# Kernel optimization log

Measured on AMD Instinct MI355X. Metric: run time of the kernel, lower is better.

The kernel has to match this reference:

```python
import jax, jax.numpy as jnp
import numpy as np

D = 64          # d_model
H = 128         # ffn_hidden_dim
N = 10000       # nodes
E = 50000       # edges
NEG_SLOPE = 0.01  # LeakyReLU default


def setup_inputs() -> dict:
    key = jax.random.key(0)
    ks = jax.random.split(key, 10)
    x = jax.random.normal(ks[0], (N, D), dtype=jnp.float32)
    edge_index = jax.random.randint(ks[1], (2, E), 0, N)
    edge_attr = jax.random.normal(ks[2], (E, D), dtype=jnp.float32)
    # MapE2NxN params (stored as [in, out] so forward is x @ W + b)
    w1 = jax.random.normal(ks[3], (D, H), dtype=jnp.float32) / np.sqrt(D)
    b1 = jnp.zeros((H,), dtype=jnp.float32)
    w2 = jax.random.normal(ks[4], (H, D * D), dtype=jnp.float32) / np.sqrt(H)
    b2 = jnp.zeros((D * D,), dtype=jnp.float32)
    # NNConv root weight + bias
    root = jax.random.normal(ks[5], (D, D), dtype=jnp.float32) / np.sqrt(D)
    bias = jnp.zeros((D,), dtype=jnp.float32)
    # LayerNorm affine params
    gamma = jnp.ones((D,), dtype=jnp.float32)
    beta = jnp.zeros((D,), dtype=jnp.float32)
    return {"x": x, "edge_attr": edge_attr, "gamma": gamma, "beta": beta,
            "w1": w1, "b1": b1, "w2": w2, "b2": b2,
            "root": root, "bias": bias, "edge_index": edge_index}


def _layer_norm(h, gamma, beta, eps=1e-5):
    mu = jnp.mean(h, axis=-1, keepdims=True)
    var = jnp.var(h, axis=-1, keepdims=True)
    return (h - mu) * jax.lax.rsqrt(var + eps) * gamma + beta


def _leaky_relu(h):
    return jnp.where(h >= 0, h, NEG_SLOPE * h)


def reference(x, edge_attr, gamma, beta, w1, b1, w2, b2, root, bias, edge_index):
    src, dst = edge_index[0], edge_index[1]
    # DeepGCNLayer block='res+': pre-activation norm -> act -> (dropout p=0) -> conv -> residual
    h = _leaky_relu(_layer_norm(x, gamma, beta))
    # MapE2NxN on edge attributes -> per-edge [D, D] weight matrix
    we = _leaky_relu(edge_attr @ w1 + b1) @ w2 + b2   # [E, D*D]
    we = we.reshape(E, D, D)
    # per-edge matvec with source node features (PyG NNConv message)
    msg = jnp.einsum('ed,edf->ef', h[src], we)        # [E, D]
    # scatter-mean aggregate into destination nodes
    agg = jax.ops.segment_sum(msg, dst, num_segments=N)
    cnt = jax.ops.segment_sum(jnp.ones((E,), dtype=msg.dtype), dst, num_segments=N)
    agg = agg / jnp.maximum(cnt, 1.0)[:, None]
    # root transform + bias, then residual
    out = agg + h @ root + bias
    return x + out
```

## Files before the change

### kernel.cpp

```cpp
#include <hip/hip_runtime.h>

#define NS 10000
#define DD 64
#define HH 128
#define EE 50000
#define SLOPE 0.01f

typedef __attribute__((ext_vector_type(8))) short short8;
typedef __attribute__((ext_vector_type(4))) float f32x4;

static __device__ __forceinline__ unsigned short f2bf(float f) {
  unsigned int u = __float_as_uint(f);
  u += 0x7fff + ((u >> 16) & 1);
  return (unsigned short)(u >> 16);
}

__device__ __forceinline__ float wave_sum64(float v) {
  #pragma unroll
  for (int m = 32; m >= 1; m >>= 1) v += __shfl_xor(v, m, 64);
  return v;
}

#define TBLK 128
__global__ __launch_bounds__(256) void k_prep(const float* __restrict__ x,
    const float* __restrict__ gamma, const float* __restrict__ beta,
    float* __restrict__ h, unsigned short* __restrict__ hbf,
    const float* __restrict__ ea, unsigned short* __restrict__ eabf,
    const float* __restrict__ w2, unsigned short* __restrict__ w2t2,
    const float* __restrict__ w1, unsigned short* __restrict__ w1t,
    const float* __restrict__ b2, unsigned short* __restrict__ b2t,
    const int* __restrict__ ei, int* __restrict__ cntsrc,
    int* __restrict__ cntdst) {
  __shared__ float tile[64][65];
  int t = threadIdx.x;
  int bid = blockIdx.x;
  if (bid < TBLK) {
    int k = bid;
    #pragma unroll
    for (int i = 0; i < 16; ++i) {
      int idx = t + i * 256;
      tile[idx >> 6][idx & 63] = w2[k * (DD * DD) + idx];
    }
    __syncthreads();
    #pragma unroll
    for (int it = 0; it < 2; ++it) {
      int slot = t + it * 256;
      int f = slot >> 3, l8 = slot & 7;
      short8 o;
      #pragma unroll
      for (int j = 0; j < 8; ++j) o[j] = f2bf(tile[l8 * 8 + j][f]);
      *(short8*)(w2t2 + ((size_t)(f * HH + k)) * DD + l8 * 8) = o;
    }
    return;
  }
  int pbid = bid - TBLK;
  int gid = pbid * 256 + t;
  if (gid < EE) {
    atomicAdd(&cntsrc[ei[gid]], 1);
    atomicAdd(&cntdst[ei[EE + gid]], 1);
  }
  if (gid < EE * DD / 8) {
    const float4* sp = (const float4*)(ea + (size_t)gid * 8);
    float4 v0 = sp[0], v1 = sp[1];
    short8 o;
    o[0] = f2bf(v0.x); o[1] = f2bf(v0.y); o[2] = f2bf(v0.z); o[3] = f2bf(v0.w);
    o[4] = f2bf(v1.x); o[5] = f2bf(v1.y); o[6] = f2bf(v1.z); o[7] = f2bf(v1.w);
    *(short8*)(eabf + (size_t)gid * 8) = o;
  }
  if (gid < DD * HH) {
    int d = gid & 63, hc = gid >> 6;
    w1t[gid] = f2bf(w1[d * HH + hc]);
  }
  if (gid < DD * DD) {
    int d = gid & 63, f = gid >> 6;
    b2t[gid] = f2bf(b2[d * DD + f]);
  }
  int wid = t >> 6;
  int lane = t & 63;
  int row = pbid * 4 + wid;
  if (row >= NS) return;
  float v = x[row * DD + lane];
  float s = wave_sum64(v);
  float s2 = wave_sum64(v * v);
  float mu = s * (1.0f / 64.0f);
  float var = s2 * (1.0f / 64.0f) - mu * mu;
  float r = rsqrtf(var + 1e-5f);
  float hn = (v - mu) * r * gamma[lane] + beta[lane];
  float hv = hn >= 0.f ? hn : SLOPE * hn;
  h[row * DD + lane] = hv;
  hbf[row * DD + lane] = f2bf(hv);
}

#define UBLK 782
#define CBLK 157
#define TSTART 944
__global__ __launch_bounds__(256) void k_midT(
    const unsigned short* __restrict__ eabf, const unsigned short* __restrict__ w1t,
    const float* __restrict__ b1, unsigned short* __restrict__ ubf,
    const unsigned short* __restrict__ hbf, const unsigned short* __restrict__ b2t,
    float* __restrict__ cc, const int* __restrict__ cntsrc,
    int* __restrict__ rowptr, int* __restrict__ cursor,
    const unsigned short* __restrict__ w2t2, unsigned short* __restrict__ T,
    int n0, int n1, int gx, int doMid) {
  __shared__ unsigned short As[64][72];
  __shared__ unsigned short Bs[128 * 72];
  int t = threadIdx.x;
  int bid = blockIdx.x;
  int w = t >> 6, lane = t & 63, lr = lane & 15, lg = lane >> 4;
  if (bid < UBLK) {
    if (!doMid) return;
    int r0 = bid * 64 + w * 16;
    int ra = r0 + lr; if (ra >= EE) ra = EE - 1;
    short8 a0 = *(const short8*)(eabf + (size_t)ra * DD + lg * 8);
    short8 a1 = *(const short8*)(eabf + (size_t)ra * DD + 32 + lg * 8);
    short8 bb0[8], bb1[8];
    #pragma unroll
    for (int ni = 0; ni < 8; ++ni) {
      const unsigned short* bp = w1t + (ni * 16 + lr) * DD;
      bb0[ni] = *(const short8*)(bp + lg * 8);
      bb1[ni] = *(const short8*)(bp + 32 + lg * 8);
    }
    f32x4 acc[8] = {};
    #pragma unroll
    for (int ni = 0; ni < 8; ++ni) {
      acc[ni] = __builtin_amdgcn_mfma_f32_16x16x32_bf16(a0, bb0[ni], acc[ni], 0, 0, 0);
      acc[ni] = __builtin_amdgcn_mfma_f32_16x16x32_bf16(a1, bb1[ni], acc[ni], 0, 0, 0);
    }
    #pragma unroll
    for (int ni = 0; ni < 8; ++ni) {
      int col = ni * 16 + lr;
      float bb = b1[col];
      #pragma unroll
      for (int reg = 0; reg < 4; ++reg) {
        int gr = r0 + lg * 4 + reg;
        if (gr < EE) {
          float vv = acc[ni][reg] + bb;
          ubf[(size_t)gr * HH + col] = f2bf(vv >= 0.f ? vv : SLOPE * vv);
        }
      }
    }
    return;
  } else if (bid < UBLK + CBLK) {
    if (!doMid) return;
    int row0 = (bid - UBLK) * 64;
    short8 a[4][2];
    #pragma unroll
    for (int mi = 0; mi < 4; ++mi) {
      int ra = row0 + mi * 16 + lr; if (ra >= NS) ra = NS - 1;
      a[mi][0] = *(const short8*)(hbf + (size_t)ra * DD + lg * 8);
      a[mi][1] = *(const short8*)(hbf + (size_t)ra * DD + 32 + lg * 8);
    }
    const unsigned short* bp = b2t + (w * 16 + lr) * DD;
    short8 b0 = *(const short8*)(bp + lg * 8);
    short8 b1v = *(const short8*)(bp + 32 + lg * 8);
    f32x4 acc[4] = {};
    #pragma unroll
    for (int mi = 0; mi < 4; ++mi) {
      acc[mi] = __builtin_amdgcn_mfma_f32_16x16x32_bf16(a[mi][0], b0, acc[mi], 0, 0, 0);
      acc[mi] = __builtin_amdgcn_mfma_f32_16x16x32_bf16(a[mi][1], b1v, acc[mi], 0, 0, 0);
    }
    #pragma unroll
    for (int mi = 0; mi < 4; ++mi)
      #pragma unroll
      for (int reg = 0; reg < 4; ++reg) {
        int gr = row0 + mi * 16 + lg * 4 + reg;
        if (gr < NS) cc[(size_t)gr * DD + w * 16 + lr] = acc[mi][reg];
      }
    return;
  } else if (bid == UBLK + CBLK) {
    if (!doMid) return;
    int* ps = (int*)&As[0][0];
    const int CH = (NS + 255) / 256;
    int base = t * CH;
    int sum = 0;
    for (int i = 0; i < CH; ++i) {
      int idx = base + i;
      if (idx < NS) sum += cntsrc[idx];
    }
    ps[t] = sum;
    __syncthreads();
    for (int off = 1; off < 256; off <<= 1) {
      int v = (t >= off) ? ps[t - off] : 0;
      __syncthreads();
      ps[t] += v;
      __syncthreads();
    }
    int run = ps[t] - sum;
    for (int i = 0; i < CH; ++i) {
      int idx = base + i;
      if (idx < NS) {
        rowptr[idx] = run;
        cursor[idx] = run;
        run += cntsrc[idx];
      }
    }
    if (t == 255) rowptr[NS] = run;
    return;
  }
  if (bid < TSTART) return;
  int tb = bid - TSTART;
  int bx = tb % gx, by = tb / gx;
  int row0 = n0 + bx * 64;
  if (row0 >= n1) return;
  int col0 = by * 128;
  #pragma unroll
  for (int i = 0; i < 2; ++i) {
    int idx = t + i * 256;
    int r = idx >> 3, cc2 = (idx & 7) * 8;
    int gr = row0 + r;
    short8 v = {};
    if (gr < n1) v = *(const short8*)(hbf + (size_t)gr * DD + cc2);
    *(short8*)(&As[r][cc2]) = v;
  }
  #pragma unroll
  for (int i = 0; i < 4; ++i) {
    int idx = t + i * 256;
    int cL = idx >> 3, rr = (idx & 7) * 8;
    int gc = col0 + cL;
    short8 v = *(const short8*)(w2t2 + (size_t)gc * DD + rr);
    *(short8*)(&Bs[cL * 72 + rr]) = v;
  }
  __syncthreads();
  f32x4 acc[4][2] = {};
  #pragma unroll
  for (int kk = 0; kk < 64; kk += 32) {
    short8 a[4], b[2];
    #pragma unroll
    for (int mi = 0; mi < 4; ++mi)
      a[mi] = *(const short8*)(&As[mi * 16 + lr][kk + lg * 8]);
    #pragma unroll
    for (int ni = 0; ni < 2; ++ni)
      b[ni] = *(const short8*)(&Bs[(w * 32 + ni * 16 + lr) * 72 + kk + lg * 8]);
    #pragma unroll
    for (int mi = 0; mi < 4; ++mi)
      #pragma unroll
      for (int ni = 0; ni < 2; ++ni)
        acc[mi][ni] = __builtin_amdgcn_mfma_f32_16x16x32_bf16(
            a[mi], b[ni], acc[mi][ni], 0, 0, 0);
  }
  __syncthreads();
  #pragma unroll
  for (int mi = 0; mi < 4; ++mi)
    #pragma unroll
    for (int ni = 0; ni < 2; ++ni) {
      int col = w * 32 + ni * 16 + lr;
      #pragma unroll
      for (int reg = 0; reg < 4; ++reg)
        Bs[(mi * 16 + lg * 4 + reg) * 132 + col] = f2bf(acc[mi][ni][reg]);
    }
  __syncthreads();
  #pragma unroll
  for (int i = 0; i < 4; ++i) {
    int idx = t + i * 256;
    int row = idx >> 4, seg = idx & 15;
    int gr = row0 + row;
    if (gr < n1) {
      short8 v = *(const short8*)(&Bs[row * 132 + seg * 8]);
      *(short8*)(T + (size_t)(gr - n0) * (HH * DD) + col0 + seg * 8) = v;
    }
  }
}

__global__ __launch_bounds__(256) void k_scatter(const int* __restrict__ ei,
    int* __restrict__ cursor, int* __restrict__ eord) {
  int e = blockIdx.x * 256 + threadIdx.x;
  if (e < EE) {
    int s = ei[e];
    int pos = atomicAdd(&cursor[s], 1);
    eord[pos] = e;
  }
}

__global__ __launch_bounds__(256) void k_msg_wave(
    const unsigned short* __restrict__ ubf, const unsigned short* __restrict__ T,
    const float* __restrict__ cc, const int* __restrict__ ei,
    const int* __restrict__ rowptr, const int* __restrict__ eord,
    float* __restrict__ agg, int n0, int n1) {
  int wid = threadIdx.x >> 6;
  int lane = threadIdx.x & 63;
  int s = n0 + blockIdx.x * 64 + blockIdx.y * 4 + wid;
  if (s >= n1) return;
  int beg = rowptr[s];
  int deg = rowptr[s + 1] - beg;
  if (deg == 0) return;
  int lr = lane & 15, lg = lane >> 4;
  int ev = 0, dv = 0;
  if (lane < 16 && lane < deg) {
    ev = eord[beg + lane];
    dv = ei[EE + ev];
  }
  const unsigned short* tp = T + (size_t)(s - n0) * (HH * DD);
  short8 b[4][4];
  #pragma unroll
  for (int ft = 0; ft < 4; ++ft)
    #pragma unroll
    for (int kk = 0; kk < 4; ++kk)
      b[ft][kk] =
          *(const short8*)(tp + (ft * 16 + lr) * HH + kk * 32 + lg * 8);
  float clv[4];
  #pragma unroll
  for (int ft = 0; ft < 4; ++ft) clv[ft] = cc[(size_t)s * DD + ft * 16 + lr];

  for (int p0 = 0; p0 < deg; p0 += 16) {
    if (p0) {
      ev = 0; dv = 0;
      if (lane < 16 && p0 + lane < deg) {
        ev = eord[beg + p0 + lane];
        dv = ei[EE + ev];
      }
    }
    int el = __shfl(ev, (p0 + lr < deg) ? lr : 0);
    const unsigned short* up = ubf + (size_t)el * HH;
    short8 au[4];
    #pragma unroll
    for (int kk = 0; kk < 4; ++kk)
      au[kk] = *(const short8*)(up + kk * 32 + lg * 8);
    f32x4 acc[4] = {};
    #pragma unroll
    for (int kk = 0; kk < 4; ++kk)
      #pragma unroll
      for (int ft = 0; ft < 4; ++ft)
        acc[ft] = __builtin_amdgcn_mfma_f32_16x16x32_bf16(au[kk], b[ft][kk],
                                                          acc[ft], 0, 0, 0);
    #pragma unroll
    for (int reg = 0; reg < 4; ++reg) {
      int eidx = p0 + lg * 4 + reg;
      int dstn = __shfl(dv, lg * 4 + reg);
      if (eidx < deg) {
        #pragma unroll
        for (int ft = 0; ft < 4; ++ft)
          atomicAdd(&agg[(size_t)dstn * DD + ft * 16 + lr],
                    acc[ft][reg] + clv[ft]);
      }
    }
  }
}

__global__ __launch_bounds__(256) void k_final(const float* __restrict__ x,
    const float* __restrict__ h, const float* __restrict__ root,
    const float* __restrict__ bias, const float* __restrict__ agg,
    const int* __restrict__ cnt, float* __restrict__ out) {
  __shared__ float Bs[DD][DD + 1];
  __shared__ float As[32][DD];
  int t = threadIdx.x;
  #pragma unroll
  for (int i = 0; i < 16; ++i) {
    int idx = t + i * 256;
    Bs[idx >> 6][idx & 63] = root[idx];
  }
  int row0 = blockIdx.x * 32;
  #pragma unroll
  for (int i = 0; i < 8; ++i) {
    int idx = t + i * 256;
    int r = idx >> 6, d = idx & 63;
    int gr = row0 + r;
    As[r][d] = (gr < NS) ? h[gr * DD + d] : 0.f;
  }
  __syncthreads();
  int r = t >> 3;
  int c0 = (t & 7) * 8;
  int gr = row0 + r;
  if (gr >= NS) return;
  float acc[8] = {};
  for (int d = 0; d < DD; ++d) {
    float a = As[r][d];
    #pragma unroll
    for (int j = 0; j < 8; ++j) acc[j] += a * Bs[d][c0 + j];
  }
  float inv = 1.0f / fmaxf((float)cnt[gr], 1.0f);
  #pragma unroll
  for (int j = 0; j < 8; ++j) {
    size_t gi = (size_t)gr * DD + c0 + j;
    out[gi] = x[gi] + agg[gi] * inv + acc[j] + bias[c0 + j];
  }
}

extern "C" void kernel_launch(void* const* d_in, const int* in_sizes, int n_in,
                              void* d_out, int out_size, void* d_ws, size_t ws_size,
                              hipStream_t stream) {
  const float* x     = (const float*)d_in[0];
  const float* ea    = (const float*)d_in[1];
  const float* gamma = (const float*)d_in[2];
  const float* beta  = (const float*)d_in[3];
  const float* w1    = (const float*)d_in[4];
  const float* b1    = (const float*)d_in[5];
  const float* w2    = (const float*)d_in[6];
  const float* b2    = (const float*)d_in[7];
  const float* root  = (const float*)d_in[8];
  const float* bias  = (const float*)d_in[9];
  const int*   ei    = (const int*)d_in[10];
  float* out = (float*)d_out;

  char* p = (char*)d_ws;
  auto carve = [&](size_t bytes) {
    char* q = p;
    p += (bytes + 255) & ~(size_t)255;
    return q;
  };
  float* h             = (float*)carve(sizeof(float) * NS * DD);
  unsigned short* hbf  = (unsigned short*)carve(sizeof(short) * NS * DD);
  float* cc            = (float*)carve(sizeof(float) * NS * DD);
  unsigned short* w2t2 = (unsigned short*)carve(sizeof(short) * HH * DD * DD);
  unsigned short* w1t  = (unsigned short*)carve(sizeof(short) * DD * HH);
  unsigned short* b2t  = (unsigned short*)carve(sizeof(short) * DD * DD);
  unsigned short* eabf = (unsigned short*)carve(sizeof(short) * (size_t)EE * DD);
  unsigned short* ubf  = (unsigned short*)carve(sizeof(short) * (size_t)EE * HH);
  int* rowptr          = (int*)carve(sizeof(int) * (NS + 1));
  int* cursor          = (int*)carve(sizeof(int) * NS);
  int* eord            = (int*)carve(sizeof(int) * EE);
  char* z0 = p;
  float* agg           = (float*)carve(sizeof(float) * NS * DD);
  int* cntdst          = (int*)carve(sizeof(int) * NS);
  int* cntsrc          = (int*)carve(sizeof(int) * NS);
  size_t zlen = (size_t)(p - z0);
  size_t fixed = (size_t)(p - (char*)d_ws);

  size_t freeb = (ws_size > fixed) ? (ws_size - fixed - 256) : 0;
  int rows = (int)(freeb / (sizeof(short) * HH * DD));
  if (rows >= NS) rows = NS;
  else { rows &= ~63; if (rows < 64) rows = 64; }
  unsigned short* Tt = (unsigned short*)carve(sizeof(short) * (size_t)rows * HH * DD);

  hipMemsetAsync(z0, 0, zlen, stream);
  k_prep<<<dim3(TBLK + (NS + 3) / 4), dim3(256), 0, stream>>>(
      x, gamma, beta, h, hbf, ea, eabf, w2, w2t2, w1, w1t, b2, b2t,
      ei, cntsrc, cntdst);

  bool first = true;
  for (int n0 = 0; n0 < NS; n0 += rows) {
    int n1 = n0 + rows;
    if (n1 > NS) n1 = NS;
    int nr = n1 - n0;
    int gx = (((nr + 63) / 64) + 7) & ~7;
    k_midT<<<dim3(TSTART + gx * (HH * DD / 128)), dim3(256), 0, stream>>>(
        eabf, w1t, b1, ubf, hbf, b2t, cc, cntsrc, rowptr, cursor,
        w2t2, Tt, n0, n1, gx, first ? 1 : 0);
    if (first)
      k_scatter<<<dim3((EE + 255) / 256), dim3(256), 0, stream>>>(ei, cursor, eord);
    k_msg_wave<<<dim3(gx, 16), dim3(256), 0, stream>>>(
        ubf, Tt, cc, ei, rowptr, eord, agg, n0, n1);
    first = false;
  }

  k_final<<<dim3((NS + 31) / 32), dim3(256), 0, stream>>>(x, h, root, bias, agg,
                                                          cntdst, out);
}
```

Measured before the change: 119.5 us.

## Overlap second-half T-tile GEMM with first-half message pass in one kernel

When the workspace holds all node T matrices, the work is split into two node chunks. A combined kernel interleaves message blocks for the first chunk with T-tile GEMM blocks for the second chunk, so the memory-bound gather/atomic work runs alongside the MFMA GEMM. A final message kernel then handles the second chunk. This adds a launch and relies on the block interleaving to balance the two kinds of work.

Result: slower. 153.3 us (+28.3%).

```diff
diff --git a/kernel.cpp b/kernel.cpp
--- a/kernel.cpp
+++ b/kernel.cpp
@@ -5,6 +5,7 @@
 #define HH 128
 #define EE 50000
 #define SLOPE 0.01f
+#define CH0 5120
 
 typedef __attribute__((ext_vector_type(8))) short short8;
 typedef __attribute__((ext_vector_type(4))) float f32x4;
@@ -20,6 +21,132 @@
   for (int m = 32; m >= 1; m >>= 1) v += __shfl_xor(v, m, 64);
   return v;
 }
+
+
+__device__ __forceinline__ void t_tile_body(
+    const unsigned short* __restrict__ hbf, const unsigned short* __restrict__ w2t2,
+    unsigned short* __restrict__ T, int n0, int n1, int row0, int col0, int t,
+    unsigned short (*As)[72], unsigned short* Bs) {
+  int w = t >> 6, lane = t & 63, lr = lane & 15, lg = lane >> 4;
+  #pragma unroll
+  for (int i = 0; i < 2; ++i) {
+    int idx = t + i * 256;
+    int r = idx >> 3, cc2 = (idx & 7) * 8;
+    int gr = row0 + r;
+    short8 v = {};
+    if (gr < n1) v = *(const short8*)(hbf + (size_t)gr * DD + cc2);
+    *(short8*)(&As[r][cc2]) = v;
+  }
+  #pragma unroll
+  for (int i = 0; i < 4; ++i) {
+    int idx = t + i * 256;
+    int cL = idx >> 3, rr = (idx & 7) * 8;
+    int gc = col0 + cL;
+    short8 v = *(const short8*)(w2t2 + (size_t)gc * DD + rr);
+    *(short8*)(&Bs[cL * 72 + rr]) = v;
+  }
+  __syncthreads();
+  f32x4 acc[4][2] = {};
+  #pragma unroll
+  for (int kk = 0; kk < 64; kk += 32) {
+    short8 a[4], b[2];
+    #pragma unroll
+    for (int mi = 0; mi < 4; ++mi)
+      a[mi] = *(const short8*)(&As[mi * 16 + lr][kk + lg * 8]);
+    #pragma unroll
+    for (int ni = 0; ni < 2; ++ni)
+      b[ni] = *(const short8*)(&Bs[(w * 32 + ni * 16 + lr) * 72 + kk + lg * 8]);
+    #pragma unroll
+    for (int mi = 0; mi < 4; ++mi)
+      #pragma unroll
+      for (int ni = 0; ni < 2; ++ni)
+        acc[mi][ni] = __builtin_amdgcn_mfma_f32_16x16x32_bf16(
+            a[mi], b[ni], acc[mi][ni], 0, 0, 0);
+  }
+  __syncthreads();
+  #pragma unroll
+  for (int mi = 0; mi < 4; ++mi)
+    #pragma unroll
+    for (int ni = 0; ni < 2; ++ni) {
+      int col = w * 32 + ni * 16 + lr;
+      #pragma unroll
+      for (int reg = 0; reg < 4; ++reg)
+        Bs[(mi * 16 + lg * 4 + reg) * 132 + col] = f2bf(acc[mi][ni][reg]);
+    }
+  __syncthreads();
+  #pragma unroll
+  for (int i = 0; i < 4; ++i) {
+    int idx = t + i * 256;
+    int row = idx >> 4, seg = idx & 15;
+    int gr = row0 + row;
+    if (gr < n1) {
+      short8 v = *(const short8*)(&Bs[row * 132 + seg * 8]);
+      *(short8*)(T + (size_t)(gr - n0) * (HH * DD) + col0 + seg * 8) = v;
+    }
+  }
+}
+
+__device__ __forceinline__ void msg_wave_body(
+    const unsigned short* __restrict__ ubf, const unsigned short* __restrict__ T,
+    const float* __restrict__ cc, const int* __restrict__ ei,
+    const int* __restrict__ rowptr, const int* __restrict__ eord,
+    float* __restrict__ agg, int s, int n0, int lane) {
+  int beg = rowptr[s];
+  int deg = rowptr[s + 1] - beg;
+  if (deg == 0) return;
+  int lr = lane & 15, lg = lane >> 4;
+  int ev = 0, dv = 0;
+  if (lane < 16 && lane < deg) {
+    ev = eord[beg + lane];
+    dv = ei[EE + ev];
+  }
+  const unsigned short* tp = T + (size_t)(s - n0) * (HH * DD);
+  short8 b[4][4];
+  #pragma unroll
+  for (int ft = 0; ft < 4; ++ft)
+    #pragma unroll
+    for (int kk = 0; kk < 4; ++kk)
+      b[ft][kk] =
+          *(const short8*)(tp + (ft * 16 + lr) * HH + kk * 32 + lg * 8);
+  float clv[4];
+  #pragma unroll
+  for (int ft = 0; ft < 4; ++ft) clv[ft] = cc[(size_t)s * DD + ft * 16 + lr];
+
+  for (int p0 = 0; p0 < deg; p0 += 16) {
+    if (p0) {
+      ev = 0; dv = 0;
+      if (lane < 16 && p0 + lane < deg) {
+        ev = eord[beg + p0 + lane];
+        dv = ei[EE + ev];
+      }
+    }
+    int el = __shfl(ev, (p0 + lr < deg) ? lr : 0);
+    const unsigned short* up = ubf + (size_t)el * HH;
+    short8 au[4];
+    #pragma unroll
+    for (int kk = 0; kk < 4; ++kk)
+      au[kk] = *(const short8*)(up + kk * 32 + lg * 8);
+    f32x4 acc[4] = {};
+    #pragma unroll
+    for (int kk = 0; kk < 4; ++kk)
+      #pragma unroll
+      for (int ft = 0; ft < 4; ++ft)
+        acc[ft] = __builtin_amdgcn_mfma_f32_16x16x32_bf16(au[kk], b[ft][kk],
+                                                          acc[ft], 0, 0, 0);
+    #pragma unroll
+    for (int reg = 0; reg < 4; ++reg) {
+      int eidx = p0 + lg * 4 + reg;
+      int dstn = __shfl(dv, lg * 4 + reg);
+      if (eidx < deg) {
+        #pragma unroll
+        for (int ft = 0; ft < 4; ++ft)
+          atomicAdd(&agg[(size_t)dstn * DD + ft * 16 + lr],
+                    acc[ft][reg] + clv[ft]);
+      }
+    }
+  }
+}
+
 
 #define TBLK 128
 __global__ __launch_bounds__(256) void k_prep(const float* __restrict__ x,
@@ -202,63 +329,7 @@
   int bx = tb % gx, by = tb / gx;
   int row0 = n0 + bx * 64;
   if (row0 >= n1) return;
-  int col0 = by * 128;
-  #pragma unroll
-  for (int i = 0; i < 2; ++i) {
-    int idx = t + i * 256;
-    int r = idx >> 3, cc2 = (idx & 7) * 8;
-    int gr = row0 + r;
-    short8 v = {};
-    if (gr < n1) v = *(const short8*)(hbf + (size_t)gr * DD + cc2);
-    *(short8*)(&As[r][cc2]) = v;
-  }
-  #pragma unroll
-  for (int i = 0; i < 4; ++i) {
-    int idx = t + i * 256;
-    int cL = idx >> 3, rr = (idx & 7) * 8;
-    int gc = col0 + cL;
-    short8 v = *(const short8*)(w2t2 + (size_t)gc * DD + rr);
-    *(short8*)(&Bs[cL * 72 + rr]) = v;
-  }
-  __syncthreads();
-  f32x4 acc[4][2] = {};
-  #pragma unroll
-  for (int kk = 0; kk < 64; kk += 32) {
-    short8 a[4], b[2];
-    #pragma unroll
-    for (int mi = 0; mi < 4; ++mi)
-      a[mi] = *(const short8*)(&As[mi * 16 + lr][kk + lg * 8]);
-    #pragma unroll
-    for (int ni = 0; ni < 2; ++ni)
-      b[ni] = *(const short8*)(&Bs[(w * 32 + ni * 16 + lr) * 72 + kk + lg * 8]);
-    #pragma unroll
-    for (int mi = 0; mi < 4; ++mi)
-      #pragma unroll
-      for (int ni = 0; ni < 2; ++ni)
-        acc[mi][ni] = __builtin_amdgcn_mfma_f32_16x16x32_bf16(
-            a[mi], b[ni], acc[mi][ni], 0, 0, 0);
-  }
-  __syncthreads();
-  #pragma unroll
-  for (int mi = 0; mi < 4; ++mi)
-    #pragma unroll
-    for (int ni = 0; ni < 2; ++ni) {
-      int col = w * 32 + ni * 16 + lr;
-      #pragma unroll
-      for (int reg = 0; reg < 4; ++reg)
-        Bs[(mi * 16 + lg * 4 + reg) * 132 + col] = f2bf(acc[mi][ni][reg]);
-    }
-  __syncthreads();
-  #pragma unroll
-  for (int i = 0; i < 4; ++i) {
-    int idx = t + i * 256;
-    int row = idx >> 4, seg = idx & 15;
-    int gr = row0 + row;
-    if (gr < n1) {
-      short8 v = *(const short8*)(&Bs[row * 132 + seg * 8]);
-      *(short8*)(T + (size_t)(gr - n0) * (HH * DD) + col0 + seg * 8) = v;
-    }
-  }
+  t_tile_body(hbf, w2t2, T, n0, n1, row0, by * 128, t, As, Bs);
 }
 
 __global__ __launch_bounds__(256) void k_scatter(const int* __restrict__ ei,
@@ -271,69 +342,43 @@
   }
 }
 
+__global__ __launch_bounds__(256) void k_Tmsg(
+    const unsigned short* __restrict__ ubf, const unsigned short* __restrict__ Tr,
+    const float* __restrict__ cc, const int* __restrict__ ei,
+    const int* __restrict__ rowptr, const int* __restrict__ eord,
+    float* __restrict__ agg,
+    const unsigned short* __restrict__ hbf, const unsigned short* __restrict__ w2t2,
+    unsigned short* __restrict__ Tw, int tn0, int tn1, int gxt, int mB) {
+  __shared__ unsigned short As[64][72];
+  __shared__ unsigned short Bs[128 * 72];
+  int t = threadIdx.x;
+  int bid = blockIdx.x;
+  int lane = t & 63;
+  int iEnd = mB * 4;
+  bool isMsg = (bid < iEnd) && ((bid & 3) == 0);
+  if (isMsg) {
+    int mb = bid >> 2;
+    int s = mb * 4 + (t >> 6);
+    if (s < CH0)
+      msg_wave_body(ubf, Tr, cc, ei, rowptr, eord, agg, s, 0, lane);
+    return;
+  }
+  int tidx = (bid < iEnd) ? (bid - (bid >> 2) - 1) : (bid - mB);
+  int bx = tidx % gxt, by = tidx / gxt;
+  int row0 = tn0 + bx * 64;
+  if (row0 >= tn1 || by >= 64) return;
+  t_tile_body(hbf, w2t2, Tw, tn0, tn1, row0, by * 128, t, As, Bs);
+}
+
 __global__ __launch_bounds__(256) void k_msg_wave(
     const unsigned short* __restrict__ ubf, const unsigned short* __restrict__ T,
     const float* __restrict__ cc, const int* __restrict__ ei,
     const int* __restrict__ rowptr, const int* __restrict__ eord,
     float* __restrict__ agg, int n0, int n1) {
-  int wid = threadIdx.x >> 6;
   int lane = threadIdx.x & 63;
-  int s = n0 + blockIdx.x * 64 + blockIdx.y * 4 + wid;
+  int s = n0 + blockIdx.x * 64 + blockIdx.y * 4 + (threadIdx.x >> 6);
   if (s >= n1) return;
-  int beg = rowptr[s];
-  int deg = rowptr[s + 1] - beg;
-  if (deg == 0) return;
-  int lr = lane & 15, lg = lane >> 4;
-  int ev = 0, dv = 0;
-  if (lane < 16 && lane < deg) {
-    ev = eord[beg + lane];
-    dv = ei[EE + ev];
-  }
-  const unsigned short* tp = T + (size_t)(s - n0) * (HH * DD);
-  short8 b[4][4];
-  #pragma unroll
-  for (int ft = 0; ft < 4; ++ft)
-    #pragma unroll
-    for (int kk = 0; kk < 4; ++kk)
-      b[ft][kk] =
-          *(const short8*)(tp + (ft * 16 + lr) * HH + kk * 32 + lg * 8);
-  float clv[4];
-  #pragma unroll
-  for (int ft = 0; ft < 4; ++ft) clv[ft] = cc[(size_t)s * DD + ft * 16 + lr];
-
-  for (int p0 = 0; p0 < deg; p0 += 16) {
-    if (p0) {
-      ev = 0; dv = 0;
-      if (lane < 16 && p0 + lane < deg) {
-        ev = eord[beg + p0 + lane];
-        dv = ei[EE + ev];
-      }
-    }
-    int el = __shfl(ev, (p0 + lr < deg) ? lr : 0);
-    const unsigned short* up = ubf + (size_t)el * HH;
-    short8 au[4];
-    #pragma unroll
-    for (int kk = 0; kk < 4; ++kk)
-      au[kk] = *(const short8*)(up + kk * 32 + lg * 8);
-    f32x4 acc[4] = {};
-    #pragma unroll
-    for (int kk = 0; kk < 4; ++kk)
-      #pragma unroll
-      for (int ft = 0; ft < 4; ++ft)
-        acc[ft] = __builtin_amdgcn_mfma_f32_16x16x32_bf16(au[kk], b[ft][kk],
-                                                          acc[ft], 0, 0, 0);
-    #pragma unroll
-    for (int reg = 0; reg < 4; ++reg) {
-      int eidx = p0 + lg * 4 + reg;
-      int dstn = __shfl(dv, lg * 4 + reg);
-      if (eidx < deg) {
-        #pragma unroll
-        for (int ft = 0; ft < 4; ++ft)
-          atomicAdd(&agg[(size_t)dstn * DD + ft * 16 + lr],
-                    acc[ft][reg] + clv[ft]);
-      }
-    }
-  }
+  msg_wave_body(ubf, T, cc, ei, rowptr, eord, agg, s, n0, lane);
 }
 
 __global__ __launch_bounds__(256) void k_final(const float* __restrict__ x,
@@ -426,20 +471,36 @@
       x, gamma, beta, h, hbf, ea, eabf, w2, w2t2, w1, w1t, b2, b2t,
       ei, cntsrc, cntdst);
 
-  bool first = true;
-  for (int n0 = 0; n0 < NS; n0 += rows) {
-    int n1 = n0 + rows;
-    if (n1 > NS) n1 = NS;
-    int nr = n1 - n0;
-    int gx = (((nr + 63) / 64) + 7) & ~7;
-    k_midT<<<dim3(TSTART + gx * (HH * DD / 128)), dim3(256), 0, stream>>>(
+  if (rows >= NS) {
+    unsigned short* Tt0 = Tt;
+    unsigned short* Tt1 = Tt + (size_t)CH0 * (HH * DD);
+    const int gx0 = CH0 / 64;
+    const int gx1 = 80;
+    k_midT<<<dim3(TSTART + gx0 * (HH * DD / 128)), dim3(256), 0, stream>>>(
         eabf, w1t, b1, ubf, hbf, b2t, cc, cntsrc, rowptr, cursor,
-        w2t2, Tt, n0, n1, gx, first ? 1 : 0);
-    if (first)
-      k_scatter<<<dim3((EE + 255) / 256), dim3(256), 0, stream>>>(ei, cursor, eord);
-    k_msg_wave<<<dim3(gx, 16), dim3(256), 0, stream>>>(
-        ubf, Tt, cc, ei, rowptr, eord, agg, n0, n1);
-    first = false;
+        w2t2, Tt0, 0, CH0, gx0, 1);
+    k_scatter<<<dim3((EE + 255) / 256), dim3(256), 0, stream>>>(ei, cursor, eord);
+    const int mB = CH0 / 4;
+    k_Tmsg<<<dim3(mB + gx1 * (HH * DD / 128)), dim3(256), 0, stream>>>(
+        ubf, Tt0, cc, ei, rowptr, eord, agg, hbf, w2t2, Tt1, CH0, NS, gx1, mB);
+    k_msg_wave<<<dim3(gx1, 16), dim3(256), 0, stream>>>(
+        ubf, Tt1, cc, ei, rowptr, eord, agg, CH0, NS);
+  } else {
+    bool first = true;
+    for (int n0 = 0; n0 < NS; n0 += rows) {
+      int n1 = n0 + rows;
+      if (n1 > NS) n1 = NS;
+      int nr = n1 - n0;
+      int gx = (((nr + 63) / 64) + 7) & ~7;
+      k_midT<<<dim3(TSTART + gx * (HH * DD / 128)), dim3(256), 0, stream>>>(
+          eabf, w1t, b1, ubf, hbf, b2t, cc, cntsrc, rowptr, cursor,
+          w2t2, Tt, n0, n1, gx, first ? 1 : 0);
+      if (first)
+        k_scatter<<<dim3((EE + 255) / 256), dim3(256), 0, stream>>>(ei, cursor, eord);
+      k_msg_wave<<<dim3(gx, 16), dim3(256), 0, stream>>>(
+          ubf, Tt, cc, ei, rowptr, eord, agg, n0, n1);
+      first = false;
+    }
   }
 
   k_final<<<dim3((NS + 31) / 32), dim3(256), 0, stream>>>(x, h, root, bias, agg,
```

## Fuse edge-attr MLP first layer into prep kernel, drop bf16 staging buffers

Applied to the files above, without the earlier changes.

Moves the edge_attr @ w1 + LeakyReLU computation out of the mid kernel into new blocks of the prep kernel. Those blocks read fp32 edge_attr directly and convert it in registers, and transpose w1 into shared memory per block. This removes the eabf and w1t intermediate buffers and their global write and read round trip, and shortens the mid kernel's grid. In exchange, every one of the 782 new blocks re-transposes the full w1 into LDS. The T-tile and message bodies are also factored into helper functions without changing behaviour.

Measured after the change: 120.7 us. No clear change (+1.0%).

```diff
diff --git a/kernel.cpp b/kernel.cpp
--- a/kernel.cpp
+++ b/kernel.cpp
@@ -21,20 +21,149 @@
   return v;
 }
 
+
+__device__ __forceinline__ void t_tile_body(
+    const unsigned short* __restrict__ hbf, const unsigned short* __restrict__ w2t2,
+    unsigned short* __restrict__ T, int n0, int n1, int row0, int col0, int t,
+    unsigned short (*As)[72], unsigned short* Bs) {
+  int w = t >> 6, lane = t & 63, lr = lane & 15, lg = lane >> 4;
+  #pragma unroll
+  for (int i = 0; i < 2; ++i) {
+    int idx = t + i * 256;
+    int r = idx >> 3, cc2 = (idx & 7) * 8;
+    int gr = row0 + r;
+    short8 v = {};
+    if (gr < n1) v = *(const short8*)(hbf + (size_t)gr * DD + cc2);
+    *(short8*)(&As[r][cc2]) = v;
+  }
+  #pragma unroll
+  for (int i = 0; i < 4; ++i) {
+    int idx = t + i * 256;
+    int cL = idx >> 3, rr = (idx & 7) * 8;
+    int gc = col0 + cL;
+    short8 v = *(const short8*)(w2t2 + (size_t)gc * DD + rr);
+    *(short8*)(&Bs[cL * 72 + rr]) = v;
+  }
+  __syncthreads();
+  f32x4 acc[4][2] = {};
+  #pragma unroll
+  for (int kk = 0; kk < 64; kk += 32) {
+    short8 a[4], b[2];
+    #pragma unroll
+    for (int mi = 0; mi < 4; ++mi)
+      a[mi] = *(const short8*)(&As[mi * 16 + lr][kk + lg * 8]);
+    #pragma unroll
+    for (int ni = 0; ni < 2; ++ni)
+      b[ni] = *(const short8*)(&Bs[(w * 32 + ni * 16 + lr) * 72 + kk + lg * 8]);
+    #pragma unroll
+    for (int mi = 0; mi < 4; ++mi)
+      #pragma unroll
+      for (int ni = 0; ni < 2; ++ni)
+        acc[mi][ni] = __builtin_amdgcn_mfma_f32_16x16x32_bf16(
+            a[mi], b[ni], acc[mi][ni], 0, 0, 0);
+  }
+  __syncthreads();
+  #pragma unroll
+  for (int mi = 0; mi < 4; ++mi)
+    #pragma unroll
+    for (int ni = 0; ni < 2; ++ni) {
+      int col = w * 32 + ni * 16 + lr;
+      #pragma unroll
+      for (int reg = 0; reg < 4; ++reg)
+        Bs[(mi * 16 + lg * 4 + reg) * 132 + col] = f2bf(acc[mi][ni][reg]);
+    }
+  __syncthreads();
+  #pragma unroll
+  for (int i = 0; i < 4; ++i) {
+    int idx = t + i * 256;
+    int row = idx >> 4, seg = idx & 15;
+    int gr = row0 + row;
+    if (gr < n1) {
+      short8 v = *(const short8*)(&Bs[row * 132 + seg * 8]);
+      *(short8*)(T + (size_t)(gr - n0) * (HH * DD) + col0 + seg * 8) = v;
+    }
+  }
+}
+
+__device__ __forceinline__ void msg_wave_body(
+    const unsigned short* __restrict__ ubf, const unsigned short* __restrict__ T,
+    const float* __restrict__ cc, const int* __restrict__ ei,
+    const int* __restrict__ rowptr, const int* __restrict__ eord,
+    float* __restrict__ agg, int s, int n0, int lane) {
+  int beg = rowptr[s];
+  int deg = rowptr[s + 1] - beg;
+  if (deg == 0) return;
+  int lr = lane & 15, lg = lane >> 4;
+  int ev = 0, dv = 0;
+  if (lane < 16 && lane < deg) {
+    ev = eord[beg + lane];
+    dv = ei[EE + ev];
+  }
+  const unsigned short* tp = T + (size_t)(s - n0) * (HH * DD);
+  short8 b[4][4];
+  #pragma unroll
+  for (int ft = 0; ft < 4; ++ft)
+    #pragma unroll
+    for (int kk = 0; kk < 4; ++kk)
+      b[ft][kk] =
+          *(const short8*)(tp + (ft * 16 + lr) * HH + kk * 32 + lg * 8);
+  float clv[4];
+  #pragma unroll
+  for (int ft = 0; ft < 4; ++ft) clv[ft] = cc[(size_t)s * DD + ft * 16 + lr];
+
+  for (int p0 = 0; p0 < deg; p0 += 16) {
+    if (p0) {
+      ev = 0; dv = 0;
+      if (lane < 16 && p0 + lane < deg) {
+        ev = eord[beg + p0 + lane];
+        dv = ei[EE + ev];
+      }
+    }
+    int el = __shfl(ev, (p0 + lr < deg) ? lr : 0);
+    const unsigned short* up = ubf + (size_t)el * HH;
+    short8 au[4];
+    #pragma unroll
+    for (int kk = 0; kk < 4; ++kk)
+      au[kk] = *(const short8*)(up + kk * 32 + lg * 8);
+    f32x4 acc[4] = {};
+    #pragma unroll
+    for (int kk = 0; kk < 4; ++kk)
+      #pragma unroll
+      for (int ft = 0; ft < 4; ++ft)
+        acc[ft] = __builtin_amdgcn_mfma_f32_16x16x32_bf16(au[kk], b[ft][kk],
+                                                          acc[ft], 0, 0, 0);
+    #pragma unroll
+    for (int reg = 0; reg < 4; ++reg) {
+      int eidx = p0 + lg * 4 + reg;
+      int dstn = __shfl(dv, lg * 4 + reg);
+      if (eidx < deg) {
+        #pragma unroll
+        for (int ft = 0; ft < 4; ++ft)
+          atomicAdd(&agg[(size_t)dstn * DD + ft * 16 + lr],
+                    acc[ft][reg] + clv[ft]);
+      }
+    }
+  }
+}
+
+
 #define TBLK 128
+#define PBLK 2500
+#define UB 782
 __global__ __launch_bounds__(256) void k_prep(const float* __restrict__ x,
     const float* __restrict__ gamma, const float* __restrict__ beta,
     float* __restrict__ h, unsigned short* __restrict__ hbf,
-    const float* __restrict__ ea, unsigned short* __restrict__ eabf,
-    const float* __restrict__ w2, unsigned short* __restrict__ w2t2,
-    const float* __restrict__ w1, unsigned short* __restrict__ w1t,
+    const float* __restrict__ ea, const float* __restrict__ w2,
+    unsigned short* __restrict__ w2t2, const float* __restrict__ w1,
+    const float* __restrict__ b1, unsigned short* __restrict__ ubf,
     const float* __restrict__ b2, unsigned short* __restrict__ b2t,
     const int* __restrict__ ei, int* __restrict__ cntsrc,
     int* __restrict__ cntdst) {
-  __shared__ float tile[64][65];
+  __shared__ __align__(16) unsigned char smem[18432];
   int t = threadIdx.x;
   int bid = blockIdx.x;
   if (bid < TBLK) {
+    float (*tile)[65] = (float(*)[65])smem;
     int k = bid;
     #pragma unroll
     for (int i = 0; i < 16; ++i) {
@@ -53,50 +182,85 @@
     }
     return;
   }
-  int pbid = bid - TBLK;
-  int gid = pbid * 256 + t;
-  if (gid < EE) {
-    atomicAdd(&cntsrc[ei[gid]], 1);
-    atomicAdd(&cntdst[ei[EE + gid]], 1);
-  }
-  if (gid < EE * DD / 8) {
-    const float4* sp = (const float4*)(ea + (size_t)gid * 8);
-    float4 v0 = sp[0], v1 = sp[1];
-    short8 o;
-    o[0] = f2bf(v0.x); o[1] = f2bf(v0.y); o[2] = f2bf(v0.z); o[3] = f2bf(v0.w);
-    o[4] = f2bf(v1.x); o[5] = f2bf(v1.y); o[6] = f2bf(v1.z); o[7] = f2bf(v1.w);
-    *(short8*)(eabf + (size_t)gid * 8) = o;
-  }
-  if (gid < DD * HH) {
-    int d = gid & 63, hc = gid >> 6;
-    w1t[gid] = f2bf(w1[d * HH + hc]);
-  }
-  if (gid < DD * DD) {
-    int d = gid & 63, f = gid >> 6;
-    b2t[gid] = f2bf(b2[d * DD + f]);
-  }
-  int wid = t >> 6;
-  int lane = t & 63;
-  int row = pbid * 4 + wid;
-  if (row >= NS) return;
-  float v = x[row * DD + lane];
-  float s = wave_sum64(v);
-  float s2 = wave_sum64(v * v);
-  float mu = s * (1.0f / 64.0f);
-  float var = s2 * (1.0f / 64.0f) - mu * mu;
-  float r = rsqrtf(var + 1e-5f);
-  float hn = (v - mu) * r * gamma[lane] + beta[lane];
-  float hv = hn >= 0.f ? hn : SLOPE * hn;
-  h[row * DD + lane] = hv;
-  hbf[row * DD + lane] = f2bf(hv);
-}
-
-#define UBLK 782
+  if (bid < TBLK + PBLK) {
+    int pbid = bid - TBLK;
+    int gid = pbid * 256 + t;
+    if (gid < EE) {
+      atomicAdd(&cntsrc[ei[gid]], 1);
+      atomicAdd(&cntdst[ei[EE + gid]], 1);
+    }
+    if (gid < DD * DD) {
+      int d = gid & 63, f = gid >> 6;
+      b2t[gid] = f2bf(b2[d * DD + f]);
+    }
+    int wid = t >> 6;
+    int lane = t & 63;
+    int row = pbid * 4 + wid;
+    if (row >= NS) return;
+    float v = x[row * DD + lane];
+    float s = wave_sum64(v);
+    float s2 = wave_sum64(v * v);
+    float mu = s * (1.0f / 64.0f);
+    float var = s2 * (1.0f / 64.0f) - mu * mu;
+    float r = rsqrtf(var + 1e-5f);
+    float hn = (v - mu) * r * gamma[lane] + beta[lane];
+    float hv = hn >= 0.f ? hn : SLOPE * hn;
+    h[row * DD + lane] = hv;
+    hbf[row * DD + lane] = f2bf(hv);
+    return;
+  }
+  int ublk = bid - TBLK - PBLK;
+  unsigned short (*W)[72] = (unsigned short(*)[72])smem;
+  int w = t >> 6, lane = t & 63, lr = lane & 15, lg = lane >> 4;
+  int r0 = ublk * 64 + w * 16;
+  int ra = r0 + lr; if (ra >= EE) ra = EE - 1;
+  const float* ep = ea + (size_t)ra * DD;
+  float4 e0 = *(const float4*)(ep + lg * 8);
+  float4 e1 = *(const float4*)(ep + lg * 8 + 4);
+  float4 e2 = *(const float4*)(ep + 32 + lg * 8);
+  float4 e3 = *(const float4*)(ep + 32 + lg * 8 + 4);
+  #pragma unroll
+  for (int i = 0; i < 32; ++i) {
+    int idx = t + i * 256;
+    int d = idx >> 7, hc = idx & 127;
+    W[hc][d] = f2bf(w1[idx]);
+  }
+  __syncthreads();
+  short8 a0, a1;
+  a0[0] = f2bf(e0.x); a0[1] = f2bf(e0.y); a0[2] = f2bf(e0.z); a0[3] = f2bf(e0.w);
+  a0[4] = f2bf(e1.x); a0[5] = f2bf(e1.y); a0[6] = f2bf(e1.z); a0[7] = f2bf(e1.w);
+  a1[0] = f2bf(e2.x); a1[1] = f2bf(e2.y); a1[2] = f2bf(e2.z); a1[3] = f2bf(e2.w);
+  a1[4] = f2bf(e3.x); a1[5] = f2bf(e3.y); a1[6] = f2bf(e3.z); a1[7] = f2bf(e3.w);
+  short8 bb0[8], bb1[8];
+  #pragma unroll
+  for (int ni = 0; ni < 8; ++ni) {
+    bb0[ni] = *(const short8*)(&W[ni * 16 + lr][lg * 8]);
+    bb1[ni] = *(const short8*)(&W[ni * 16 + lr][32 + lg * 8]);
+  }
+  f32x4 acc[8] = {};
+  #pragma unroll
+  for (int ni = 0; ni < 8; ++ni) {
+    acc[ni] = __builtin_amdgcn_mfma_f32_16x16x32_bf16(a0, bb0[ni], acc[ni], 0, 0, 0);
+    acc[ni] = __builtin_amdgcn_mfma_f32_16x16x32_bf16(a1, bb1[ni], acc[ni], 0, 0, 0);
+  }
+  #pragma unroll
+  for (int ni = 0; ni < 8; ++ni) {
+    int col = ni * 16 + lr;
+    float bb = b1[col];
+    #pragma unroll
+    for (int reg = 0; reg < 4; ++reg) {
+      int gr = r0 + lg * 4 + reg;
+      if (gr < EE) {
+        float vv = acc[ni][reg] + bb;
+        ubf[(size_t)gr * HH + col] = f2bf(vv >= 0.f ? vv : SLOPE * vv);
+      }
+    }
+  }
+}
+
 #define CBLK 157
-#define TSTART 944
-__global__ __launch_bounds__(256) void k_midT(
-    const unsigned short* __restrict__ eabf, const unsigned short* __restrict__ w1t,
-    const float* __restrict__ b1, unsigned short* __restrict__ ubf,
+#define TSTART2 160
+__global__ __launch_bounds__(256) void k_ccT(
     const unsigned short* __restrict__ hbf, const unsigned short* __restrict__ b2t,
     float* __restrict__ cc, const int* __restrict__ cntsrc,
     int* __restrict__ rowptr, int* __restrict__ cursor,
@@ -107,42 +271,9 @@
   int t = threadIdx.x;
   int bid = blockIdx.x;
   int w = t >> 6, lane = t & 63, lr = lane & 15, lg = lane >> 4;
-  if (bid < UBLK) {
+  if (bid < CBLK) {
     if (!doMid) return;
-    int r0 = bid * 64 + w * 16;
-    int ra = r0 + lr; if (ra >= EE) ra = EE - 1;
-    short8 a0 = *(const short8*)(eabf + (size_t)ra * DD + lg * 8);
-    short8 a1 = *(const short8*)(eabf + (size_t)ra * DD + 32 + lg * 8);
-    short8 bb0[8], bb1[8];
-    #pragma unroll
-    for (int ni = 0; ni < 8; ++ni) {
-      const unsigned short* bp = w1t + (ni * 16 + lr) * DD;
-      bb0[ni] = *(const short8*)(bp + lg * 8);
-      bb1[ni] = *(const short8*)(bp + 32 + lg * 8);
-    }
-    f32x4 acc[8] = {};
-    #pragma unroll
-    for (int ni = 0; ni < 8; ++ni) {
-      acc[ni] = __builtin_amdgcn_mfma_f32_16x16x32_bf16(a0, bb0[ni], acc[ni], 0, 0, 0);
-      acc[ni] = __builtin_amdgcn_mfma_f32_16x16x32_bf16(a1, bb1[ni], acc[ni], 0, 0, 0);
-    }
-    #pragma unroll
-    for (int ni = 0; ni < 8; ++ni) {
-      int col = ni * 16 + lr;
-      float bb = b1[col];
-      #pragma unroll
-      for (int reg = 0; reg < 4; ++reg) {
-        int gr = r0 + lg * 4 + reg;
-        if (gr < EE) {
-          float vv = acc[ni][reg] + bb;
-          ubf[(size_t)gr * HH + col] = f2bf(vv >= 0.f ? vv : SLOPE * vv);
-        }
-      }
-    }
-    return;
-  } else if (bid < UBLK + CBLK) {
-    if (!doMid) return;
-    int row0 = (bid - UBLK) * 64;
+    int row0 = bid * 64;
     short8 a[4][2];
     #pragma unroll
     for (int mi = 0; mi < 4; ++mi) {
@@ -167,7 +298,7 @@
         if (gr < NS) cc[(size_t)gr * DD + w * 16 + lr] = acc[mi][reg];
       }
     return;
-  } else if (bid == UBLK + CBLK) {
+  } else if (bid == CBLK) {
     if (!doMid) return;
     int* ps = (int*)&As[0][0];
     const int CH = (NS + 255) / 256;
@@ -197,68 +328,12 @@
     if (t == 255) rowptr[NS] = run;
     return;
   }
-  if (bid < TSTART) return;
-  int tb = bid - TSTART;
+  if (bid < TSTART2) return;
+  int tb = bid - TSTART2;
   int bx = tb % gx, by = tb / gx;
   int row0 = n0 + bx * 64;
   if (row0 >= n1) return;
-  int col0 = by * 128;
-  #pragma unroll
-  for (int i = 0; i < 2; ++i) {
-    int idx = t + i * 256;
-    int r = idx >> 3, cc2 = (idx & 7) * 8;
-    int gr = row0 + r;
-    short8 v = {};
-    if (gr < n1) v = *(const short8*)(hbf + (size_t)gr * DD + cc2);
-    *(short8*)(&As[r][cc2]) = v;
-  }
-  #pragma unroll
-  for (int i = 0; i < 4; ++i) {
-    int idx = t + i * 256;
-    int cL = idx >> 3, rr = (idx & 7) * 8;
-    int gc = col0 + cL;
-    short8 v = *(const short8*)(w2t2 + (size_t)gc * DD + rr);
-    *(short8*)(&Bs[cL * 72 + rr]) = v;
-  }
-  __syncthreads();
-  f32x4 acc[4][2] = {};
-  #pragma unroll
-  for (int kk = 0; kk < 64; kk += 32) {
-    short8 a[4], b[2];
-    #pragma unroll
-    for (int mi = 0; mi < 4; ++mi)
-      a[mi] = *(const short8*)(&As[mi * 16 + lr][kk + lg * 8]);
-    #pragma unroll
-    for (int ni = 0; ni < 2; ++ni)
-      b[ni] = *(const short8*)(&Bs[(w * 32 + ni * 16 + lr) * 72 + kk + lg * 8]);
-    #pragma unroll
-    for (int mi = 0; mi < 4; ++mi)
-      #pragma unroll
-      for (int ni = 0; ni < 2; ++ni)
-        acc[mi][ni] = __builtin_amdgcn_mfma_f32_16x16x32_bf16(
-            a[mi], b[ni], acc[mi][ni], 0, 0, 0);
-  }
-  __syncthreads();
-  #pragma unroll
-  for (int mi = 0; mi < 4; ++mi)
-    #pragma unroll
-    for (int ni = 0; ni < 2; ++ni) {
-      int col = w * 32 + ni * 16 + lr;
-      #pragma unroll
-      for (int reg = 0; reg < 4; ++reg)
-        Bs[(mi * 16 + lg * 4 + reg) * 132 + col] = f2bf(acc[mi][ni][reg]);
-    }
-  __syncthreads();
-  #pragma unroll
-  for (int i = 0; i < 4; ++i) {
-    int idx = t + i * 256;
-    int row = idx >> 4, seg = idx & 15;
-    int gr = row0 + row;
-    if (gr < n1) {
-      short8 v = *(const short8*)(&Bs[row * 132 + seg * 8]);
-      *(short8*)(T + (size_t)(gr - n0) * (HH * DD) + col0 + seg * 8) = v;
-    }
-  }
+  t_tile_body(hbf, w2t2, T, n0, n1, row0, by * 128, t, As, Bs);
 }
 
 __global__ __launch_bounds__(256) void k_scatter(const int* __restrict__ ei,
@@ -276,64 +351,10 @@
     const float* __restrict__ cc, const int* __restrict__ ei,
     const int* __restrict__ rowptr, const int* __restrict__ eord,
     float* __restrict__ agg, int n0, int n1) {
-  int wid = threadIdx.x >> 6;
   int lane = threadIdx.x & 63;
-  int s = n0 + blockIdx.x * 64 + blockIdx.y * 4 + wid;
+  int s = n0 + blockIdx.x * 64 + blockIdx.y * 4 + (threadIdx.x >> 6);
   if (s >= n1) return;
-  int beg = rowptr[s];
-  int deg = rowptr[s + 1] - beg;
-  if (deg == 0) return;
-  int lr = lane & 15, lg = lane >> 4;
-  int ev = 0, dv = 0;
-  if (lane < 16 && lane < deg) {
-    ev = eord[beg + lane];
-    dv = ei[EE + ev];
-  }
-  const unsigned short* tp = T + (size_t)(s - n0) * (HH * DD);
-  short8 b[4][4];
-  #pragma unroll
-  for (int ft = 0; ft < 4; ++ft)
-    #pragma unroll
-    for (int kk = 0; kk < 4; ++kk)
-      b[ft][kk] =
-          *(const short8*)(tp + (ft * 16 + lr) * HH + kk * 32 + lg * 8);
-  float clv[4];
-  #pragma unroll
-  for (int ft = 0; ft < 4; ++ft) clv[ft] = cc[(size_t)s * DD + ft * 16 + lr];
-
-  for (int p0 = 0; p0 < deg; p0 += 16) {
-    if (p0) {
-      ev = 0; dv = 0;
-      if (lane < 16 && p0 + lane < deg) {
-        ev = eord[beg + p0 + lane];
-        dv = ei[EE + ev];
-      }
-    }
-    int el = __shfl(ev, (p0 + lr < deg) ? lr : 0);
-    const unsigned short* up = ubf + (size_t)el * HH;
-    short8 au[4];
-    #pragma unroll
-    for (int kk = 0; kk < 4; ++kk)
-      au[kk] = *(const short8*)(up + kk * 32 + lg * 8);
-    f32x4 acc[4] = {};
-    #pragma unroll
-    for (int kk = 0; kk < 4; ++kk)
-      #pragma unroll
-      for (int ft = 0; ft < 4; ++ft)
-        acc[ft] = __builtin_amdgcn_mfma_f32_16x16x32_bf16(au[kk], b[ft][kk],
-                                                          acc[ft], 0, 0, 0);
-    #pragma unroll
-    for (int reg = 0; reg < 4; ++reg) {
-      int eidx = p0 + lg * 4 + reg;
-      int dstn = __shfl(dv, lg * 4 + reg);
-      if (eidx < deg) {
-        #pragma unroll
-        for (int ft = 0; ft < 4; ++ft)
-          atomicAdd(&agg[(size_t)dstn * DD + ft * 16 + lr],
-                    acc[ft][reg] + clv[ft]);
-      }
-    }
-  }
+  msg_wave_body(ubf, T, cc, ei, rowptr, eord, agg, s, n0, lane);
 }
 
 __global__ __launch_bounds__(256) void k_final(const float* __restrict__ x,
@@ -401,9 +422,7 @@
   unsigned short* hbf  = (unsigned short*)carve(sizeof(short) * NS * DD);
   float* cc            = (float*)carve(sizeof(float) * NS * DD);
   unsigned short* w2t2 = (unsigned short*)carve(sizeof(short) * HH * DD * DD);
-  unsigned short* w1t  = (unsigned short*)carve(sizeof(short) * DD * HH);
   unsigned short* b2t  = (unsigned short*)carve(sizeof(short) * DD * DD);
-  unsigned short* eabf = (unsigned short*)carve(sizeof(short) * (size_t)EE * DD);
   unsigned short* ubf  = (unsigned short*)carve(sizeof(short) * (size_t)EE * HH);
   int* rowptr          = (int*)carve(sizeof(int) * (NS + 1));
   int* cursor          = (int*)carve(sizeof(int) * NS);
@@ -422,8 +441,8 @@
   unsigned short* Tt = (unsigned short*)carve(sizeof(short) * (size_t)rows * HH * DD);
 
   hipMemsetAsync(z0, 0, zlen, stream);
-  k_prep<<<dim3(TBLK + (NS + 3) / 4), dim3(256), 0, stream>>>(
-      x, gamma, beta, h, hbf, ea, eabf, w2, w2t2, w1, w1t, b2, b2t,
+  k_prep<<<dim3(TBLK + PBLK + UB), dim3(256), 0, stream>>>(
+      x, gamma, beta, h, hbf, ea, w2, w2t2, w1, b1, ubf, b2, b2t,
       ei, cntsrc, cntdst);
 
   bool first = true;
@@ -432,9 +451,9 @@
     if (n1 > NS) n1 = NS;
     int nr = n1 - n0;
     int gx = (((nr + 63) / 64) + 7) & ~7;
-    k_midT<<<dim3(TSTART + gx * (HH * DD / 128)), dim3(256), 0, stream>>>(
-        eabf, w1t, b1, ubf, hbf, b2t, cc, cntsrc, rowptr, cursor,
-        w2t2, Tt, n0, n1, gx, first ? 1 : 0);
+    k_ccT<<<dim3(TSTART2 + gx * (HH * DD / 128)), dim3(256), 0, stream>>>(
+        hbf, b2t, cc, cntsrc, rowptr, cursor, w2t2, Tt, n0, n1, gx,
+        first ? 1 : 0);
     if (first)
       k_scatter<<<dim3((EE + 255) / 256), dim3(256), 0, stream>>>(ei, cursor, eord);
     k_msg_wave<<<dim3(gx, 16), dim3(256), 0, stream>>>(
```
